# Performance work log

Hardware: AMD Instinct MI355X
Metric: run time of the kernel (lower is better)

Reference implementation:

```python
import jax, jax.numpy as jnp
import numpy as np

TAU = 0.25
VTH = 1.0

def setup_inputs() -> dict:
    key = jax.random.key(0)
    k1, k2 = jax.random.split(key)
    B, T, F, U = 256, 100, 1024, 1024
    x = jax.random.normal(k1, (B, T, F), dtype=jnp.float32)
    kernel = jax.random.normal(k2, (F, U), dtype=jnp.float32) * 0.02
    bias = jnp.zeros((U,), dtype=jnp.float32)
    return {"x": x, "kernel": kernel, "bias": bias}

def reference(x, kernel, bias):
    # x: [B, T, F]; one big GEMM for all timesteps, then sequential LIF scan.
    current = jnp.einsum('btf,fu->btu', x, kernel) + bias  # [B, T, U]
    B, T, U = current.shape
    v0 = jnp.zeros((B, U), dtype=x.dtype)

    def lif_step(voltage, cur_t):
        voltage = TAU * voltage + (1.0 - TAU) * cur_t
        spikes = (voltage > VTH).astype(cur_t.dtype)
        voltage = voltage - spikes * VTH
        return voltage, spikes

    _, spikes_t = jax.lax.scan(lif_step, v0, jnp.moveaxis(current, 1, 0))  # [T, B, U]
    output_spikes = jnp.moveaxis(spikes_t, 0, 1)  # [B, T, U]
    spike_counts = jnp.sum(output_spikes, axis=1)  # [B, U]
    return output_spikes, spike_counts
```

## Files before the change

### kernel.cpp

```cpp
#include <hip/hip_runtime.h>


#define UN 128
#define BK 16
#define CS 132
#define CHUNK 50
#define TMAX 100

__device__ __forceinline__ void gload_lds16(const float* g, float* l) {
    __builtin_amdgcn_global_load_lds(
        (const __attribute__((address_space(1))) void*)g,
        (__attribute__((address_space(3))) void*)l,
        16, 0, 0);
}

__global__ __launch_bounds__(256) void fused_snn(
    const float* __restrict__ x,
    const float* __restrict__ W,
    const float* __restrict__ bias,
    float* __restrict__ spikes,
    float* __restrict__ counts,
    int B, int T, int F, int U)
{
    __shared__ __align__(16) float smem[CHUNK * CS];
    float* As0 = smem;
    float* As1 = smem + 1600;

    const int tid = threadIdx.x;
    const int tg  = tid >> 4;
    const int ug  = tid & 15;
    const int u0  = blockIdx.x * UN;
    const int b   = blockIdx.y;

    float acc[7][8];
    #pragma unroll
    for (int i = 0; i < 7; i++)
        #pragma unroll
        for (int j = 0; j < 8; j++) acc[i][j] = 0.f;

    const float* xb = x + (size_t)b * T * F;

    const float* ga0 = xb + (size_t)(tid >> 2) * F + (tid & 3) * 4;
    const float* ga1 = xb + (size_t)(64 + (tid >> 2)) * F + (tid & 3) * 4;
    const int la0 = tid * 4;
    const int la1 = (256 + tid) * 4;
    const bool a1on = (tid < 144);
    const bool w0   = (tid < 64);

    const float* wlane = W + u0 + 4 * ug;

#define STAGE(buf, kof)                                   \
    do {                                                  \
        gload_lds16(ga0 + (kof), (buf) + la0);            \
        if (a1on) gload_lds16(ga1 + (kof), (buf) + la1);  \
    } while (0)

#define COMPUTE(buf, k0b)                                                  \
    do {                                                                   \
        const float* ap = (buf) + tg * 16;                                 \
        _Pragma("unroll 1")                                                \
        for (int kk = 0; kk < BK; kk += 2) {                               \
            const int kn = ((k0b) + kk + 2 < F) ? ((k0b) + kk + 2) : 0;    \
            const float* wn = wlane + (size_t)kn * U;                      \
            float4 n0 = *(const float4*)(wn);                              \
            float4 n1 = *(const float4*)(wn + 64);                         \
            float4 n2 = *(const float4*)(wn + U);                          \
            float4 n3 = *(const float4*)(wn + U + 64);                     \
            _Pragma("unroll")                                              \
            for (int i = 0; i < 6; i++) {                                  \
                float2 a = *(const float2*)(ap + i * 256 + kk);            \
                acc[i][0] += a.x * c0.x;  acc[i][1] += a.x * c0.y;         \
                acc[i][2] += a.x * c0.z;  acc[i][3] += a.x * c0.w;         \
                acc[i][4] += a.x * c1.x;  acc[i][5] += a.x * c1.y;         \
                acc[i][6] += a.x * c1.z;  acc[i][7] += a.x * c1.w;         \
                acc[i][0] += a.y * c2.x;  acc[i][1] += a.y * c2.y;         \
                acc[i][2] += a.y * c2.z;  acc[i][3] += a.y * c2.w;         \
                acc[i][4] += a.y * c3.x;  acc[i][5] += a.y * c3.y;         \
                acc[i][6] += a.y * c3.z;  acc[i][7] += a.y * c3.w;         \
            }                                                              \
            if (w0) {     \
                float2 a = *(const float2*)(ap + 6 * 256 + kk);            \
                acc[6][0] += a.x * c0.x;  acc[6][1] += a.x * c0.y;         \
                acc[6][2] += a.x * c0.z;  acc[6][3] += a.x * c0.w;         \
                acc[6][4] += a.x * c1.x;  acc[6][5] += a.x * c1.y;         \
                acc[6][6] += a.x * c1.z;  acc[6][7] += a.x * c1.w;         \
                acc[6][0] += a.y * c2.x;  acc[6][1] += a.y * c2.y;         \
                acc[6][2] += a.y * c2.z;  acc[6][3] += a.y * c2.w;         \
                acc[6][4] += a.y * c3.x;  acc[6][5] += a.y * c3.y;         \
                acc[6][6] += a.y * c3.z;  acc[6][7] += a.y * c3.w;         \
            }                                                              \
            c0 = n0; c1 = n1; c2 = n2; c3 = n3;                            \
        }                                                                  \
    } while (0)

    STAGE(As0, 0);
    float4 c0 = *(const float4*)(wlane);
    float4 c1 = *(const float4*)(wlane + 64);
    float4 c2 = *(const float4*)(wlane + U);
    float4 c3 = *(const float4*)(wlane + U + 64);
    __syncthreads();

    #pragma unroll 1
    for (int k0 = 0; k0 < F; k0 += 2 * BK) {
        STAGE(As1, k0 + BK);
        COMPUTE(As0, k0);
        __syncthreads();
        if (k0 + 2 * BK < F) STAGE(As0, k0 + 2 * BK);
        COMPUTE(As1, k0 + BK);
        __syncthreads();
    }

#undef STAGE
#undef COMPUTE

    float bb[8];
    {
        float4 bv0 = *(const float4*)(bias + u0 + 4 * ug);
        float4 bv1 = *(const float4*)(bias + u0 + 64 + 4 * ug);
        bb[0] = bv0.x; bb[1] = bv0.y; bb[2] = bv0.z; bb[3] = bv0.w;
        bb[4] = bv1.x; bb[5] = bv1.y; bb[6] = bv1.z; bb[7] = bv1.w;
    }

    float v = 0.f, cnt = 0.f;
    float* sp = spikes + (size_t)b * T * U + u0 + tid;

    #pragma unroll
    for (int c = 0; c < 2; c++) {
        #pragma unroll
        for (int i = 0; i < 7; i++) {
            const int t = i * 16 + tg;
            if (t >= c * CHUNK && t < c * CHUNK + CHUNK && t < TMAX) {
                const int r = t - c * CHUNK;
                float4 d0, d1;
                d0.x = acc[i][0] + bb[0]; d0.y = acc[i][1] + bb[1];
                d0.z = acc[i][2] + bb[2]; d0.w = acc[i][3] + bb[3];
                d1.x = acc[i][4] + bb[4]; d1.y = acc[i][5] + bb[5];
                d1.z = acc[i][6] + bb[6]; d1.w = acc[i][7] + bb[7];
                *(float4*)(smem + r * CS + 4 * ug)      = d0;
                *(float4*)(smem + r * CS + 64 + 4 * ug) = d1;
            }
        }
        __syncthreads();
        if (tid < UN) {
#pragma clang fp contract(off)
            for (int r = 0; r < CHUNK; r++) {
                float cval = smem[r * CS + tid];
                v = 0.25f * v + 0.75f * cval;
                float s = (v > 1.0f) ? 1.0f : 0.0f;
                v -= s;
                cnt += s;
                sp[(size_t)(c * CHUNK + r) * U] = s;
            }
        }
        __syncthreads();
    }
    if (tid < UN) counts[(size_t)b * U + u0 + tid] = cnt;
}

extern "C" void kernel_launch(void* const* d_in, const int* in_sizes, int n_in,
                              void* d_out, int out_size, void* d_ws, size_t ws_size,
                              hipStream_t stream) {
    const float* x    = (const float*)d_in[0];
    const float* kern = (const float*)d_in[1];
    const float* bias = (const float*)d_in[2];
    float* out = (float*)d_out;

    const int U = in_sizes[2];
    const int F = in_sizes[1] / U;
    const int R = in_sizes[0] / F;
    const int B = out_size / U - R;
    const int T = R / B;

    float* spikes = out;
    float* counts = out + (size_t)R * U;

    dim3 grid(U / UN, B);
    fused_snn<<<grid, 256, 0, stream>>>(x, kern, bias, spikes, counts,
                                        B, T, F, U);
}
```

Measured before the change: 818.8 us.

## Stage weight tiles through LDS and double-buffer register fragments in the FMA loop

The weight tile is now loaded asynchronously into LDS alongside the activation tile, using the same double-buffered global_load_lds staging, instead of every thread reading W directly from global memory each k step. The inner loop is restructured to prefetch the next A and W register fragments from LDS while the current ones are being multiplied. The goal is to replace redundant global W loads with shared LDS reads and to hide LDS latency. In exchange, LDS use per block rises and more registers are held for the prefetched fragments, which may lower occupancy.

```diff
diff --git a/kernel.cpp b/kernel.cpp
--- a/kernel.cpp
+++ b/kernel.cpp
@@ -22,9 +22,11 @@
     float* __restrict__ counts,
     int B, int T, int F, int U)
 {
-    __shared__ __align__(16) float smem[CHUNK * CS];
+    __shared__ __align__(16) float smem[7296];
     float* As0 = smem;
-    float* As1 = smem + 1600;
+    float* Ws0 = smem + 1600;
+    float* As1 = smem + 3648;
+    float* Ws1 = smem + 5248;
 
     const int tid = threadIdx.x;
     const int tg  = tid >> 4;
@@ -47,71 +49,100 @@
     const bool a1on = (tid < 144);
     const bool w0   = (tid < 64);
 
-    const float* wlane = W + u0 + 4 * ug;
-
-#define STAGE(buf, kof)                                   \
-    do {                                                  \
-        gload_lds16(ga0 + (kof), (buf) + la0);            \
-        if (a1on) gload_lds16(ga1 + (kof), (buf) + la1);  \
-    } while (0)
-
-#define COMPUTE(buf, k0b)                                                  \
-    do {                                                                   \
-        const float* ap = (buf) + tg * 16;                                 \
-        _Pragma("unroll 1")                                                \
-        for (int kk = 0; kk < BK; kk += 2) {                               \
-            const int kn = ((k0b) + kk + 2 < F) ? ((k0b) + kk + 2) : 0;    \
-            const float* wn = wlane + (size_t)kn * U;                      \
-            float4 n0 = *(const float4*)(wn);                              \
-            float4 n1 = *(const float4*)(wn + 64);                         \
-            float4 n2 = *(const float4*)(wn + U);                          \
-            float4 n3 = *(const float4*)(wn + U + 64);                     \
-            _Pragma("unroll")                                              \
-            for (int i = 0; i < 6; i++) {                                  \
-                float2 a = *(const float2*)(ap + i * 256 + kk);            \
-                acc[i][0] += a.x * c0.x;  acc[i][1] += a.x * c0.y;         \
-                acc[i][2] += a.x * c0.z;  acc[i][3] += a.x * c0.w;         \
-                acc[i][4] += a.x * c1.x;  acc[i][5] += a.x * c1.y;         \
-                acc[i][6] += a.x * c1.z;  acc[i][7] += a.x * c1.w;         \
-                acc[i][0] += a.y * c2.x;  acc[i][1] += a.y * c2.y;         \
-                acc[i][2] += a.y * c2.z;  acc[i][3] += a.y * c2.w;         \
-                acc[i][4] += a.y * c3.x;  acc[i][5] += a.y * c3.y;         \
-                acc[i][6] += a.y * c3.z;  acc[i][7] += a.y * c3.w;         \
-            }                                                              \
-            if (w0) {     \
-                float2 a = *(const float2*)(ap + 6 * 256 + kk);            \
-                acc[6][0] += a.x * c0.x;  acc[6][1] += a.x * c0.y;         \
-                acc[6][2] += a.x * c0.z;  acc[6][3] += a.x * c0.w;         \
-                acc[6][4] += a.x * c1.x;  acc[6][5] += a.x * c1.y;         \
-                acc[6][6] += a.x * c1.z;  acc[6][7] += a.x * c1.w;         \
-                acc[6][0] += a.y * c2.x;  acc[6][1] += a.y * c2.y;         \
-                acc[6][2] += a.y * c2.z;  acc[6][3] += a.y * c2.w;         \
-                acc[6][4] += a.y * c3.x;  acc[6][5] += a.y * c3.y;         \
-                acc[6][6] += a.y * c3.z;  acc[6][7] += a.y * c3.w;         \
-            }                                                              \
-            c0 = n0; c1 = n1; c2 = n2; c3 = n3;                            \
-        }                                                                  \
-    } while (0)
-
-    STAGE(As0, 0);
-    float4 c0 = *(const float4*)(wlane);
-    float4 c1 = *(const float4*)(wlane + 64);
-    float4 c2 = *(const float4*)(wlane + U);
-    float4 c3 = *(const float4*)(wlane + U + 64);
+    const float* gw0 = W + (size_t)(tid >> 5) * U + u0 + (tid & 31) * 4;
+    const float* gw1 = W + (size_t)(8 + (tid >> 5)) * U + u0 + (tid & 31) * 4;
+    const int lw0 = tid * 4;
+    const int lw1 = (256 + tid) * 4;
+
+#define STAGE(abuf, wbuf, kof)                                     \
+    do {                                                           \
+        gload_lds16(ga0 + (kof), (abuf) + la0);                    \
+        if (a1on) gload_lds16(ga1 + (kof), (abuf) + la1);          \
+        gload_lds16(gw0 + (size_t)(kof) * U, (wbuf) + lw0);        \
+        gload_lds16(gw1 + (size_t)(kof) * U, (wbuf) + lw1);        \
+    } while (0)
+
+#define FMAROW(i, A, W0, W1, W2, W3)                                        \
+    do {                                                                    \
+        acc[i][0] += A.x * W0.x;  acc[i][1] += A.x * W0.y;                  \
+        acc[i][2] += A.x * W0.z;  acc[i][3] += A.x * W0.w;                  \
+        acc[i][4] += A.x * W1.x;  acc[i][5] += A.x * W1.y;                  \
+        acc[i][6] += A.x * W1.z;  acc[i][7] += A.x * W1.w;                  \
+        acc[i][0] += A.y * W2.x;  acc[i][1] += A.y * W2.y;                  \
+        acc[i][2] += A.y * W2.z;  acc[i][3] += A.y * W2.w;                  \
+        acc[i][4] += A.y * W3.x;  acc[i][5] += A.y * W3.y;                  \
+        acc[i][6] += A.y * W3.z;  acc[i][7] += A.y * W3.w;                  \
+    } while (0)
+
+#define LOADA(dst0,dst1,dst2,dst3,dst4,dst5,dst6, koff)                     \
+    do {                                                                    \
+        dst0 = *(const float2*)(ap + 0 * 256 + (koff));                     \
+        dst1 = *(const float2*)(ap + 1 * 256 + (koff));                     \
+        dst2 = *(const float2*)(ap + 2 * 256 + (koff));                     \
+        dst3 = *(const float2*)(ap + 3 * 256 + (koff));                     \
+        dst4 = *(const float2*)(ap + 4 * 256 + (koff));                     \
+        dst5 = *(const float2*)(ap + 5 * 256 + (koff));                     \
+        if (w0) dst6 = *(const float2*)(ap + 6 * 256 + (koff));             \
+    } while (0)
+
+#define LOADW(d0,d1,d2,d3, koff)                                            \
+    do {                                                                    \
+        d0 = *(const float4*)(wp + (koff) * 128);                           \
+        d1 = *(const float4*)(wp + (koff) * 128 + 64);                      \
+        d2 = *(const float4*)(wp + ((koff) + 1) * 128);                     \
+        d3 = *(const float4*)(wp + ((koff) + 1) * 128 + 64);                \
+    } while (0)
+
+#define FMASET(A0,A1,A2,A3,A4,A5,A6, W0,W1,W2,W3)                           \
+    do {                                                                    \
+        FMAROW(0, A0, W0, W1, W2, W3);                                      \
+        FMAROW(1, A1, W0, W1, W2, W3);                                      \
+        FMAROW(2, A2, W0, W1, W2, W3);                                      \
+        FMAROW(3, A3, W0, W1, W2, W3);                                      \
+        FMAROW(4, A4, W0, W1, W2, W3);                                      \
+        FMAROW(5, A5, W0, W1, W2, W3);                                      \
+        if (w0) { FMAROW(6, A6, W0, W1, W2, W3); }                          \
+    } while (0)
+
+#define COMPUTE(abuf, wbuf)                                                 \
+    do {                                                                    \
+        const float* ap = (abuf) + tg * 16;                                 \
+        const float* wp = (wbuf) + ug * 4;                                  \
+        float2 cA0,cA1,cA2,cA3,cA4,cA5,cA6, nA0,nA1,nA2,nA3,nA4,nA5,nA6;    \
+        float4 cW0,cW1,cW2,cW3, nW0,nW1,nW2,nW3;                            \
+        LOADA(cA0,cA1,cA2,cA3,cA4,cA5,cA6, 0);                              \
+        LOADW(cW0,cW1,cW2,cW3, 0);                                          \
+        _Pragma("unroll 1")                                                 \
+        for (int kk = 0; kk < BK; kk += 4) {                                \
+            LOADA(nA0,nA1,nA2,nA3,nA4,nA5,nA6, kk + 2);                     \
+            LOADW(nW0,nW1,nW2,nW3, kk + 2);                                 \
+            FMASET(cA0,cA1,cA2,cA3,cA4,cA5,cA6, cW0,cW1,cW2,cW3);           \
+            const int k4 = (kk + 4) & 15;     \
+            LOADA(cA0,cA1,cA2,cA3,cA4,cA5,cA6, k4);                         \
+            LOADW(cW0,cW1,cW2,cW3, k4);                                     \
+            FMASET(nA0,nA1,nA2,nA3,nA4,nA5,nA6, nW0,nW1,nW2,nW3);           \
+        }                                                                   \
+    } while (0)
+
+    STAGE(As0, Ws0, 0);
     __syncthreads();
 
     #pragma unroll 1
     for (int k0 = 0; k0 < F; k0 += 2 * BK) {
-        STAGE(As1, k0 + BK);
-        COMPUTE(As0, k0);
-        __syncthreads();
-        if (k0 + 2 * BK < F) STAGE(As0, k0 + 2 * BK);
-        COMPUTE(As1, k0 + BK);
+        STAGE(As1, Ws1, k0 + BK);
+        COMPUTE(As0, Ws0);
+        __syncthreads();
+        if (k0 + 2 * BK < F) STAGE(As0, Ws0, k0 + 2 * BK);
+        COMPUTE(As1, Ws1);
         __syncthreads();
     }
 
 #undef STAGE
 #undef COMPUTE
+#undef FMASET
+#undef LOADA
+#undef LOADW
+#undef FMAROW
 
     float bb[8];
     {
```

After: 891.1 us. +8.8%, slower.
